# Kernel optimization log

Hardware: AMD Instinct MI355X
Metric: run time of the kernel (lower is better)

Reference implementation:

```python
import jax, jax.numpy as jnp
import numpy as np


def setup_inputs() -> dict:
    key = jax.random.key(0)
    ks = jax.random.split(key, 6)
    B, N, D, A = 4, 512, 768, 128
    matrix = jax.random.normal(ks[0], (B, N, D), dtype=jnp.float32)
    mask = jax.random.randint(ks[1], (B, N, N, 1), 0, 2, dtype=jnp.int32)
    W1_w = jax.random.normal(ks[2], (D, A), dtype=jnp.float32) * (1.0 / np.sqrt(D))
    W1_b = jnp.zeros((A,), dtype=jnp.float32)
    W2_w = jax.random.normal(ks[3], (D, A), dtype=jnp.float32) * (1.0 / np.sqrt(D))
    W2_b = jnp.zeros((A,), dtype=jnp.float32)
    v_w = jax.random.normal(ks[4], (A, 1), dtype=jnp.float32) * (1.0 / np.sqrt(A))
    return {"matrix": matrix, "mask": mask, "W1_w": W1_w, "W1_b": W1_b,
            "W2_w": W2_w, "W2_b": W2_b, "v_w": v_w}


def reference(matrix, mask, W1_w, W1_b, W2_w, W2_b, v_w):
    # matrix: [B,N,D]; mask: [B,N,N,1]
    w1 = matrix @ W1_w + W1_b                     # [B,N,A] (query-side proj)
    w2 = matrix @ W2_w + W2_b                     # [B,N,A] (key-side proj)
    # pairwise additive scores: v . tanh(w1_i + w2_j) -> [B,N,N]
    pair = jnp.tanh(w1[:, :, None, :] + w2[:, None, :, :])  # [B,N,N,A]
    scores = jnp.einsum('bija,ao->bij', pair, v_w)           # [B,N,N]
    boolean_mask = mask[..., 0].astype(bool)                  # [B,N,N]
    neg = jnp.finfo(scores.dtype).min
    masked = jnp.where(boolean_mask, scores, neg)
    attn = jax.nn.softmax(masked, axis=-1)
    attn = jnp.where(jnp.isnan(attn), jnp.zeros((), attn.dtype), attn)
    return attn @ matrix                          # [B,N,D]
```

## Files before the change

### kernel.cpp

```cpp
#include <hip/hip_runtime.h>

#define B_ 4
#define N_ 512
#define D_ 768
#define A_ 128

typedef short bf16x8 __attribute__((ext_vector_type(8)));
typedef ushort u16x8 __attribute__((ext_vector_type(8)));
typedef float f32x4 __attribute__((ext_vector_type(4)));

__device__ __forceinline__ ushort f2h(float x) {
  uint u = __builtin_bit_cast(uint, x);
  return (ushort)((u + 0x7fffu + ((u >> 16) & 1u)) >> 16);
}
__device__ __forceinline__ float h2f(ushort h) {
  uint u = ((uint)h) << 16;
  return __builtin_bit_cast(float, u);
}
__device__ __forceinline__ bf16x8 ld8(const ushort* p) {
  return *(const bf16x8*)p;
}
#define MFMA(a, b, c) __builtin_amdgcn_mfma_f32_16x16x32_bf16(a, b, c, 0, 0, 0)

__global__ __launch_bounds__(256) void k0_prep(
    const float* __restrict__ M, const float* __restrict__ W1,
    const float* __restrict__ W2, ushort* __restrict__ Mr_h,
    ushort* __restrict__ Mr_l, ushort* __restrict__ Mt_h,
    ushort* __restrict__ Mt_l, ushort* __restrict__ Wt_h,
    ushort* __restrict__ Wt_l) {
  __shared__ ushort lds_h[64][40];
  __shared__ ushort lds_l[64][40];
  const int t = threadIdx.x;
  const int bid = blockIdx.x;
  if (bid < 768) {
    const int dq = bid % 12;
    const int rest = bid / 12;
    const int d0 = dq * 64;
    const int n0 = (rest & 15) * 32;
    const int b = rest >> 4;
    const int n = t >> 3;
    const int dg = (t & 7) * 8;
    const size_t roff = ((size_t)(b * N_ + n0 + n)) * D_ + d0 + dg;
    const float4 v0 = *(const float4*)(M + roff);
    const float4 v1 = *(const float4*)(M + roff + 4);
    const float x[8] = {v0.x, v0.y, v0.z, v0.w, v1.x, v1.y, v1.z, v1.w};
    u16x8 vh, vl;
#pragma unroll
    for (int e = 0; e < 8; ++e) {
      ushort h = f2h(x[e]);
      ushort l = f2h(x[e] - h2f(h));
      vh[e] = h;
      vl[e] = l;
      lds_h[dg + e][n] = h;
      lds_l[dg + e][n] = l;
    }
    *(u16x8*)(Mr_h + roff) = vh;
    *(u16x8*)(Mr_l + roff) = vl;
    __syncthreads();
    const int dd = t >> 2;
    const int ng = (t & 3) * 8;
    const size_t toff = ((size_t)b * D_ + d0 + dd) * N_ + n0 + ng;
    *(u16x8*)(Mt_h + toff) = *(const u16x8*)(&lds_h[dd][ng]);
    *(u16x8*)(Mt_l + toff) = *(const u16x8*)(&lds_l[dd][ng]);
  } else {
    const int c = t;
    const int k0 = (bid - 768) * 8;
    const float* __restrict__ Wp = (c < A_) ? W1 : W2;
    const int cc = c & (A_ - 1);
    u16x8 vh, vl;
#pragma unroll
    for (int e = 0; e < 8; ++e) {
      float x = Wp[(size_t)(k0 + e) * A_ + cc];
      ushort h = f2h(x);
      vh[e] = h;
      vl[e] = f2h(x - h2f(h));
    }
    *(u16x8*)(Wt_h + (size_t)c * D_ + k0) = vh;
    *(u16x8*)(Wt_l + (size_t)c * D_ + k0) = vl;
  }
}

__global__ __launch_bounds__(256) void k1_mfma(
    const ushort* __restrict__ Mr_h, const ushort* __restrict__ Mr_l,
    const ushort* __restrict__ Wt_h, const ushort* __restrict__ Wt_l,
    const float* __restrict__ b1, const float* __restrict__ b2,
    float* __restrict__ w1e, float* __restrict__ w2e) {
  __shared__ float l_red[4][32][33];
  const int t = threadIdx.x;
  const int l = t & 63;
  const int w = t >> 6;
  const int r = l & 15, g = l >> 4;
  const int row0 = blockIdx.x * 32;
  const int cb = blockIdx.y * 32;
  const int kbase = w * 192;
  const size_t oA = (size_t)(row0 + r) * D_ + kbase + g * 8;
  const size_t oA2 = oA + (size_t)16 * D_;
  const size_t oB = (size_t)(cb + r) * D_ + kbase + g * 8;
  const size_t oB2 = oB + (size_t)16 * D_;
  f32x4 acc[2][2] = {};
  bf16x8 A[2][4], Bv[2][4];
#define K1LOAD(s, k0)                                                        \
  A[s][0] = ld8(Mr_h + oA + (k0));  A[s][1] = ld8(Mr_h + oA2 + (k0));        \
  A[s][2] = ld8(Mr_l + oA + (k0));  A[s][3] = ld8(Mr_l + oA2 + (k0));        \
  Bv[s][0] = ld8(Wt_h + oB + (k0)); Bv[s][1] = ld8(Wt_h + oB2 + (k0));       \
  Bv[s][2] = ld8(Wt_l + oB + (k0)); Bv[s][3] = ld8(Wt_l + oB2 + (k0));
#define K1MM(s)                                                              \
  acc[0][0] = MFMA(A[s][0], Bv[s][0], acc[0][0]);                            \
  acc[0][0] = MFMA(A[s][0], Bv[s][2], acc[0][0]);                            \
  acc[0][0] = MFMA(A[s][2], Bv[s][0], acc[0][0]);                            \
  acc[0][1] = MFMA(A[s][0], Bv[s][1], acc[0][1]);                            \
  acc[0][1] = MFMA(A[s][0], Bv[s][3], acc[0][1]);                            \
  acc[0][1] = MFMA(A[s][2], Bv[s][1], acc[0][1]);                            \
  acc[1][0] = MFMA(A[s][1], Bv[s][0], acc[1][0]);                            \
  acc[1][0] = MFMA(A[s][1], Bv[s][2], acc[1][0]);                            \
  acc[1][0] = MFMA(A[s][3], Bv[s][0], acc[1][0]);                            \
  acc[1][1] = MFMA(A[s][1], Bv[s][1], acc[1][1]);                            \
  acc[1][1] = MFMA(A[s][1], Bv[s][3], acc[1][1]);                            \
  acc[1][1] = MFMA(A[s][3], Bv[s][1], acc[1][1]);
  K1LOAD(0, 0)
#pragma unroll
  for (int kt = 0; kt < 6; ++kt) {
    if (kt & 1) {
      if (kt < 5) { K1LOAD(0, (kt + 1) * 32) }
      K1MM(1)
    } else {
      if (kt < 5) { K1LOAD(1, (kt + 1) * 32) }
      K1MM(0)
    }
  }
#undef K1LOAD
#undef K1MM
#pragma unroll
  for (int fi = 0; fi < 2; ++fi)
#pragma unroll
    for (int fj = 0; fj < 2; ++fj)
#pragma unroll
      for (int rr = 0; rr < 4; ++rr)
        l_red[w][fi * 16 + g * 4 + rr][fj * 16 + r] = acc[fi][fj][rr];
  __syncthreads();

  const float SC = 2.8853900817779268f;
  const int b = row0 >> 9;
  const int n0 = row0 & (N_ - 1);
  if (cb < A_) {
#pragma unroll
    for (int k = 0; k < 4; ++k) {
      const int row = (t >> 5) + k * 8;
      const int col = t & 31;
      float v = l_red[0][row][col] + l_red[1][row][col] +
                l_red[2][row][col] + l_red[3][row][col];
      v = (v + b1[cb + col]) * SC;
      w1e[(size_t)(row0 + row) * A_ + cb + col] = __builtin_amdgcn_exp2f(v);
    }
  } else {
#pragma unroll
    for (int k = 0; k < 4; ++k) {
      const int row = t & 31;
      const int col = (t >> 5) + k * 8;
      float v = l_red[0][row][col] + l_red[1][row][col] +
                l_red[2][row][col] + l_red[3][row][col];
      v = (v + b2[cb - A_ + col]) * SC;
      w2e[(size_t)(b * A_ + cb - A_ + col) * N_ + n0 + row] =
          __builtin_amdgcn_exp2f(v);
    }
  }
}

__global__ __launch_bounds__(512) void k2_scores(
    const float* __restrict__ w1e, const float* __restrict__ w2e,
    const int* __restrict__ mask, const float* __restrict__ vw,
    ushort* __restrict__ ah, ushort* __restrict__ al) {
  __shared__ float l_w2[2][A_][64];
  __shared__ float l_e1[8][A_];
  __shared__ float l_v2[A_];
  const int t = threadIdx.x;
  const int lane = t & 63;
  const int w = t >> 6;
  const int i0 = blockIdx.x * 8;
  const int b = i0 >> 9;
  const int i = i0 + w;

  for (int k = t; k < 8 * A_; k += 512)
    l_e1[k >> 7][k & 127] = w1e[(size_t)(i0 + (k >> 7)) * A_ + (k & 127)];
  if (t < A_) l_v2[t] = -2.f * vw[t];
  float vs = vw[lane] + vw[64 + lane];
#pragma unroll
  for (int off = 32; off; off >>= 1) vs += __shfl_xor(vs, off);

  const float* __restrict__ w2src = w2e + (size_t)b * A_ * N_;
  float4 st[4];

#define STAGE_LOAD(jt)                                                      \
  {                                                                         \
    const int j0 = (jt) * 64;                                               \
    _Pragma("unroll") for (int k = 0; k < 4; ++k) {                         \
      const int f = t + k * 512;                                            \
      const int a = f >> 4;                                                 \
      const int j4 = (f & 15) * 4;                                          \
      st[k] = *(const float4*)(w2src + (size_t)a * N_ + j0 + j4);           \
    }                                                                       \
  }
#define STAGE_WRITE(bf)                                                     \
  {                                                                         \
    _Pragma("unroll") for (int k = 0; k < 4; ++k) {                         \
      const int f = t + k * 512;                                            \
      const int a = f >> 4;                                                 \
      const int j4 = (f & 15) * 4;                                          \
      *(float4*)(&l_w2[bf][a][j4]) = st[k];                                 \
    }                                                                       \
  }

  STAGE_LOAD(0)
  STAGE_WRITE(0)
  __syncthreads();

  const float4* __restrict__ e1q = (const float4*)&l_e1[w][0];
  const float4* __restrict__ v2q = (const float4*)&l_v2[0];
  const float NEG = -3.402823466e38f;
  float s[8];
#pragma unroll
  for (int jt = 0; jt < 8; ++jt) {
    if (jt + 1 < 8) STAGE_LOAD(jt + 1)
    const int mk = mask[(size_t)i * N_ + jt * 64 + lane];
    const float(*wb)[64] = l_w2[jt & 1];
    float acc = vs;
#pragma unroll 4
    for (int c = 0; c < 32; ++c) {
      const float4 wa = e1q[c];
      const float4 vv = v2q[c];
      const float x0 = wb[c * 4 + 0][lane];
      const float x1 = wb[c * 4 + 1][lane];
      const float x2 = wb[c * 4 + 2][lane];
      const float x3 = wb[c * 4 + 3][lane];
      const float g0 = fmaf(wa.x, x0, 1.f);
      const float g1 = fmaf(wa.y, x1, 1.f);
      const float g2 = fmaf(wa.z, x2, 1.f);
      const float g3 = fmaf(wa.w, x3, 1.f);
      acc = fmaf(vv.x, __builtin_amdgcn_rcpf(g0), acc);
      acc = fmaf(vv.y, __builtin_amdgcn_rcpf(g1), acc);
      acc = fmaf(vv.z, __builtin_amdgcn_rcpf(g2), acc);
      acc = fmaf(vv.w, __builtin_amdgcn_rcpf(g3), acc);
    }
    s[jt] = mk ? acc : NEG;
    if (jt + 1 < 8) { STAGE_WRITE((jt + 1) & 1) }
    __syncthreads();
  }
#undef STAGE_LOAD
#undef STAGE_WRITE

  float rmax = s[0];
#pragma unroll
  for (int jt = 1; jt < 8; ++jt) rmax = fmaxf(rmax, s[jt]);
#pragma unroll
  for (int off = 32; off; off >>= 1) rmax = fmaxf(rmax, __shfl_xor(rmax, off));
  const float L2E = 1.4426950408889634f;
  float psum = 0.f;
#pragma unroll
  for (int jt = 0; jt < 8; ++jt) {
    s[jt] = __builtin_amdgcn_exp2f((s[jt] - rmax) * L2E);
    psum += s[jt];
  }
#pragma unroll
  for (int off = 32; off; off >>= 1) psum += __shfl_xor(psum, off);
  const float inv = __builtin_amdgcn_rcpf(psum);
#pragma unroll
  for (int jt = 0; jt < 8; ++jt) {
    const float pv = s[jt] * inv;
    const ushort hh = f2h(pv);
    ah[(size_t)i * N_ + jt * 64 + lane] = hh;
    al[(size_t)i * N_ + jt * 64 + lane] = f2h(pv - h2f(hh));
  }
}

__global__ __launch_bounds__(256) void k3_mfma(
    const ushort* __restrict__ ah, const ushort* __restrict__ al,
    const ushort* __restrict__ Mt_h, const ushort* __restrict__ Mt_l,
    float* __restrict__ out) {
  __shared__ float l_red[4][32][33];
  const int t = threadIdx.x;
  const int l = t & 63;
  const int w = t >> 6;
  const int r = l & 15, g = l >> 4;
  const int row0 = blockIdx.x * 32;
  const int d0 = blockIdx.y * 32;
  const int b = row0 >> 9;
  const int jbase = w * 128;
  const ushort* __restrict__ Bh = Mt_h + (size_t)b * D_ * N_;
  const ushort* __restrict__ Bl = Mt_l + (size_t)b * D_ * N_;
  const size_t oA = (size_t)(row0 + r) * N_ + jbase + g * 8;
  const size_t oA2 = oA + (size_t)16 * N_;
  const size_t oB = (size_t)(d0 + r) * N_ + jbase + g * 8;
  const size_t oB2 = oB + (size_t)16 * N_;
  f32x4 acc[2][2] = {};
  bf16x8 A[2][4], Bv[2][4];
#define K3LOAD(s, j0)                                                        \
  A[s][0] = ld8(ah + oA + (j0));  A[s][1] = ld8(ah + oA2 + (j0));            \
  A[s][2] = ld8(al + oA + (j0));  A[s][3] = ld8(al + oA2 + (j0));            \
  Bv[s][0] = ld8(Bh + oB + (j0)); Bv[s][1] = ld8(Bh + oB2 + (j0));           \
  Bv[s][2] = ld8(Bl + oB + (j0)); Bv[s][3] = ld8(Bl + oB2 + (j0));
#define K3MM(s)                                                              \
  acc[0][0] = MFMA(A[s][0], Bv[s][0], acc[0][0]);                            \
  acc[0][0] = MFMA(A[s][0], Bv[s][2], acc[0][0]);                            \
  acc[0][0] = MFMA(A[s][2], Bv[s][0], acc[0][0]);                            \
  acc[0][1] = MFMA(A[s][0], Bv[s][1], acc[0][1]);                            \
  acc[0][1] = MFMA(A[s][0], Bv[s][3], acc[0][1]);                            \
  acc[0][1] = MFMA(A[s][2], Bv[s][1], acc[0][1]);                            \
  acc[1][0] = MFMA(A[s][1], Bv[s][0], acc[1][0]);                            \
  acc[1][0] = MFMA(A[s][1], Bv[s][2], acc[1][0]);                            \
  acc[1][0] = MFMA(A[s][3], Bv[s][0], acc[1][0]);                            \
  acc[1][1] = MFMA(A[s][1], Bv[s][1], acc[1][1]);                            \
  acc[1][1] = MFMA(A[s][1], Bv[s][3], acc[1][1]);                            \
  acc[1][1] = MFMA(A[s][3], Bv[s][1], acc[1][1]);
  K3LOAD(0, 0)
#pragma unroll
  for (int kt = 0; kt < 4; ++kt) {
    if (kt & 1) {
      if (kt < 3) { K3LOAD(0, (kt + 1) * 32) }
      K3MM(1)
    } else {
      if (kt < 3) { K3LOAD(1, (kt + 1) * 32) }
      K3MM(0)
    }
  }
#undef K3LOAD
#undef K3MM
#pragma unroll
  for (int fi = 0; fi < 2; ++fi)
#pragma unroll
    for (int fd = 0; fd < 2; ++fd)
#pragma unroll
      for (int rr = 0; rr < 4; ++rr)
        l_red[w][fi * 16 + g * 4 + rr][fd * 16 + r] = acc[fi][fd][rr];
  __syncthreads();
#pragma unroll
  for (int k = 0; k < 4; ++k) {
    const int row = (t >> 5) + k * 8;
    const int col = t & 31;
    const float v = l_red[0][row][col] + l_red[1][row][col] +
                    l_red[2][row][col] + l_red[3][row][col];
    out[(size_t)(row0 + row) * D_ + d0 + col] = v;
  }
}

extern "C" void kernel_launch(void* const* d_in, const int* in_sizes, int n_in,
                              void* d_out, int out_size, void* d_ws,
                              size_t ws_size, hipStream_t stream) {
  const float* M = (const float*)d_in[0];
  const int* mask = (const int*)d_in[1];
  const float* W1 = (const float*)d_in[2];
  const float* b1 = (const float*)d_in[3];
  const float* W2 = (const float*)d_in[4];
  const float* b2 = (const float*)d_in[5];
  const float* vw = (const float*)d_in[6];
  float* out = (float*)d_out;

  float* w1e = (float*)d_ws;
  float* w2e = w1e + 2048 * A_;
  ushort* ah = (ushort*)(w2e + 4 * A_ * N_);
  ushort* al = ah + 2048 * N_;
  ushort* Mr_h = al + 2048 * N_;
  ushort* Mr_l = Mr_h + 2048 * D_;
  ushort* Mt_h = Mr_l + 2048 * D_;
  ushort* Mt_l = Mt_h + 2048 * D_;
  ushort* Wt_h = Mt_l + 2048 * D_;
  ushort* Wt_l = Wt_h + 256 * D_;

  k0_prep<<<864, 256, 0, stream>>>(M, W1, W2, Mr_h, Mr_l, Mt_h, Mt_l,
                                   Wt_h, Wt_l);
  k1_mfma<<<dim3(2048 / 32, 8), 256, 0, stream>>>(Mr_h, Mr_l, Wt_h, Wt_l,
                                                  b1, b2, w1e, w2e);
  k2_scores<<<(B_ * N_) / 8, 512, 0, stream>>>(w1e, w2e, mask, vw, ah, al);
  k3_mfma<<<dim3(2048 / 32, D_ / 32), 256, 0, stream>>>(ah, al, Mt_h, Mt_l,
                                                        out);
}
```

Measured before the change: 74.80 us.

## Read w1/v rows via scalar loads in scores kernel; enlarge attn@M row tile to 64

In the scores kernel, the per-row w1e and v vectors are no longer staged through shared memory. They are read directly with a wave-uniform (readfirstlane) pointer so the compiler can use scalar loads, and the -2 scale of v is folded into the final fmaf. The attn@matrix MFMA kernel now computes 64 rows per block instead of 32, which halves the grid and reuses each B-fragment load across twice as many rows. In exchange it uses more registers and a larger shared-memory reduction buffer, which may lower occupancy.

```diff
diff --git a/kernel.cpp b/kernel.cpp
--- a/kernel.cpp
+++ b/kernel.cpp
@@ -171,18 +171,15 @@
     const int* __restrict__ mask, const float* __restrict__ vw,
     ushort* __restrict__ ah, ushort* __restrict__ al) {
   __shared__ float l_w2[2][A_][64];
-  __shared__ float l_e1[8][A_];
-  __shared__ float l_v2[A_];
   const int t = threadIdx.x;
   const int lane = t & 63;
   const int w = t >> 6;
   const int i0 = blockIdx.x * 8;
   const int b = i0 >> 9;
   const int i = i0 + w;
-
-  for (int k = t; k < 8 * A_; k += 512)
-    l_e1[k >> 7][k & 127] = w1e[(size_t)(i0 + (k >> 7)) * A_ + (k & 127)];
-  if (t < A_) l_v2[t] = -2.f * vw[t];
+  const int iu = __builtin_amdgcn_readfirstlane(i);
+  const float* __restrict__ w1row = w1e + (size_t)iu * A_;
+
   float vs = vw[lane] + vw[64 + lane];
 #pragma unroll
   for (int off = 32; off; off >>= 1) vs += __shfl_xor(vs, off);
@@ -214,8 +211,6 @@
   STAGE_WRITE(0)
   __syncthreads();
 
-  const float4* __restrict__ e1q = (const float4*)&l_e1[w][0];
-  const float4* __restrict__ v2q = (const float4*)&l_v2[0];
   const float NEG = -3.402823466e38f;
   float s[8];
 #pragma unroll
@@ -223,11 +218,11 @@
     if (jt + 1 < 8) STAGE_LOAD(jt + 1)
     const int mk = mask[(size_t)i * N_ + jt * 64 + lane];
     const float(*wb)[64] = l_w2[jt & 1];
-    float acc = vs;
+    float acc2 = 0.f;
 #pragma unroll 4
     for (int c = 0; c < 32; ++c) {
-      const float4 wa = e1q[c];
-      const float4 vv = v2q[c];
+      const float4 wa = *(const float4*)(w1row + c * 4);
+      const float4 vv = *(const float4*)(vw + c * 4);
       const float x0 = wb[c * 4 + 0][lane];
       const float x1 = wb[c * 4 + 1][lane];
       const float x2 = wb[c * 4 + 2][lane];
@@ -236,12 +231,12 @@
       const float g1 = fmaf(wa.y, x1, 1.f);
       const float g2 = fmaf(wa.z, x2, 1.f);
       const float g3 = fmaf(wa.w, x3, 1.f);
-      acc = fmaf(vv.x, __builtin_amdgcn_rcpf(g0), acc);
-      acc = fmaf(vv.y, __builtin_amdgcn_rcpf(g1), acc);
-      acc = fmaf(vv.z, __builtin_amdgcn_rcpf(g2), acc);
-      acc = fmaf(vv.w, __builtin_amdgcn_rcpf(g3), acc);
-    }
-    s[jt] = mk ? acc : NEG;
+      acc2 = fmaf(vv.x, __builtin_amdgcn_rcpf(g0), acc2);
+      acc2 = fmaf(vv.y, __builtin_amdgcn_rcpf(g1), acc2);
+      acc2 = fmaf(vv.z, __builtin_amdgcn_rcpf(g2), acc2);
+      acc2 = fmaf(vv.w, __builtin_amdgcn_rcpf(g3), acc2);
+    }
+    s[jt] = mk ? fmaf(-2.f, acc2, vs) : NEG;
     if (jt + 1 < 8) { STAGE_WRITE((jt + 1) & 1) }
     __syncthreads();
   }
@@ -276,41 +271,39 @@
     const ushort* __restrict__ ah, const ushort* __restrict__ al,
     const ushort* __restrict__ Mt_h, const ushort* __restrict__ Mt_l,
     float* __restrict__ out) {
-  __shared__ float l_red[4][32][33];
+  __shared__ float l_red[4][64][33];
   const int t = threadIdx.x;
   const int l = t & 63;
   const int w = t >> 6;
   const int r = l & 15, g = l >> 4;
-  const int row0 = blockIdx.x * 32;
+  const int row0 = blockIdx.x * 64;
   const int d0 = blockIdx.y * 32;
   const int b = row0 >> 9;
   const int jbase = w * 128;
   const ushort* __restrict__ Bh = Mt_h + (size_t)b * D_ * N_;
   const ushort* __restrict__ Bl = Mt_l + (size_t)b * D_ * N_;
-  const size_t oA = (size_t)(row0 + r) * N_ + jbase + g * 8;
-  const size_t oA2 = oA + (size_t)16 * N_;
+  size_t oA[4];
+#pragma unroll
+  for (int fi = 0; fi < 4; ++fi)
+    oA[fi] = (size_t)(row0 + fi * 16 + r) * N_ + jbase + g * 8;
   const size_t oB = (size_t)(d0 + r) * N_ + jbase + g * 8;
   const size_t oB2 = oB + (size_t)16 * N_;
-  f32x4 acc[2][2] = {};
-  bf16x8 A[2][4], Bv[2][4];
+  f32x4 acc[4][2] = {};
+  bf16x8 A[2][8], Bv[2][4];
 #define K3LOAD(s, j0)                                                        \
-  A[s][0] = ld8(ah + oA + (j0));  A[s][1] = ld8(ah + oA2 + (j0));            \
-  A[s][2] = ld8(al + oA + (j0));  A[s][3] = ld8(al + oA2 + (j0));            \
-  Bv[s][0] = ld8(Bh + oB + (j0)); Bv[s][1] = ld8(Bh + oB2 + (j0));           \
-  Bv[s][2] = ld8(Bl + oB + (j0)); Bv[s][3] = ld8(Bl + oB2 + (j0));
+  A[s][0] = ld8(ah + oA[0] + (j0)); A[s][1] = ld8(ah + oA[1] + (j0));        \
+  A[s][2] = ld8(ah + oA[2] + (j0)); A[s][3] = ld8(ah + oA[3] + (j0));        \
+  A[s][4] = ld8(al + oA[0] + (j0)); A[s][5] = ld8(al + oA[1] + (j0));        \
+  A[s][6] = ld8(al + oA[2] + (j0)); A[s][7] = ld8(al + oA[3] + (j0));        \
+  Bv[s][0] = ld8(Bh + oB + (j0));   Bv[s][1] = ld8(Bh + oB2 + (j0));         \
+  Bv[s][2] = ld8(Bl + oB + (j0));   Bv[s][3] = ld8(Bl + oB2 + (j0));
 #define K3MM(s)                                                              \
-  acc[0][0] = MFMA(A[s][0], Bv[s][0], acc[0][0]);                            \
-  acc[0][0] = MFMA(A[s][0], Bv[s][2], acc[0][0]);                            \
-  acc[0][0] = MFMA(A[s][2], Bv[s][0], acc[0][0]);                            \
-  acc[0][1] = MFMA(A[s][0], Bv[s][1], acc[0][1]);                            \
-  acc[0][1] = MFMA(A[s][0], Bv[s][3], acc[0][1]);                            \
-  acc[0][1] = MFMA(A[s][2], Bv[s][1], acc[0][1]);                            \
-  acc[1][0] = MFMA(A[s][1], Bv[s][0], acc[1][0]);                            \
-  acc[1][0] = MFMA(A[s][1], Bv[s][2], acc[1][0]);                            \
-  acc[1][0] = MFMA(A[s][3], Bv[s][0], acc[1][0]);                            \
-  acc[1][1] = MFMA(A[s][1], Bv[s][1], acc[1][1]);                            \
-  acc[1][1] = MFMA(A[s][1], Bv[s][3], acc[1][1]);                            \
-  acc[1][1] = MFMA(A[s][3], Bv[s][1], acc[1][1]);
+  _Pragma("unroll") for (int fi = 0; fi < 4; ++fi)                           \
+  _Pragma("unroll") for (int fd = 0; fd < 2; ++fd) {                         \
+    acc[fi][fd] = MFMA(A[s][fi], Bv[s][fd], acc[fi][fd]);                    \
+    acc[fi][fd] = MFMA(A[s][fi], Bv[s][fd + 2], acc[fi][fd]);                \
+    acc[fi][fd] = MFMA(A[s][fi + 4], Bv[s][fd], acc[fi][fd]);                \
+  }
   K3LOAD(0, 0)
 #pragma unroll
   for (int kt = 0; kt < 4; ++kt) {
@@ -325,7 +318,7 @@
 #undef K3LOAD
 #undef K3MM
 #pragma unroll
-  for (int fi = 0; fi < 2; ++fi)
+  for (int fi = 0; fi < 4; ++fi)
 #pragma unroll
     for (int fd = 0; fd < 2; ++fd)
 #pragma unroll
@@ -333,7 +326,7 @@
         l_red[w][fi * 16 + g * 4 + rr][fd * 16 + r] = acc[fi][fd][rr];
   __syncthreads();
 #pragma unroll
-  for (int k = 0; k < 4; ++k) {
+  for (int k = 0; k < 8; ++k) {
     const int row = (t >> 5) + k * 8;
     const int col = t & 31;
     const float v = l_red[0][row][col] + l_red[1][row][col] +
@@ -370,6 +363,6 @@
   k1_mfma<<<dim3(2048 / 32, 8), 256, 0, stream>>>(Mr_h, Mr_l, Wt_h, Wt_l,
                                                   b1, b2, w1e, w2e);
   k2_scores<<<(B_ * N_) / 8, 512, 0, stream>>>(w1e, w2e, mask, vw, ah, al);
-  k3_mfma<<<dim3(2048 / 32, D_ / 32), 256, 0, stream>>>(ah, al, Mt_h, Mt_l,
+  k3_mfma<<<dim3(2048 / 64, D_ / 32), 256, 0, stream>>>(ah, al, Mt_h, Mt_l,
                                                         out);
 }
```

After: 69.29 us. -7.4%, faster.
